# Performance work log

Measured on AMD Instinct MI355X. Metric: run time of the kernel, lower is better.

Reference implementation:

```python
import jax, jax.numpy as jnp
import numpy as np

EMBED_DIM = 1024
NUM_HEADS = 16
HEAD_DIM = EMBED_DIM // NUM_HEADS


def setup_inputs() -> dict:
    key = jax.random.key(0)
    k1, k2, k3, k4, k5 = jax.random.split(key, 5)
    B, S, D = 2, 2048, EMBED_DIM
    s_in = 1.0 / np.sqrt(D)
    x = jax.random.normal(k1, (B, S, D), dtype=jnp.float32)
    W_qkv = jax.random.uniform(k2, (D, 3 * D), dtype=jnp.float32, minval=-s_in, maxval=s_in)
    b_qkv = jax.random.uniform(k3, (3 * D,), dtype=jnp.float32, minval=-s_in, maxval=s_in)
    W_out = jax.random.uniform(k4, (D, D), dtype=jnp.float32, minval=-s_in, maxval=s_in)
    b_out = jax.random.uniform(k5, (D,), dtype=jnp.float32, minval=-s_in, maxval=s_in)
    return {"x": x, "W_qkv": W_qkv, "b_qkv": b_qkv, "W_out": W_out, "b_out": b_out}


def reference(x, W_qkv, b_qkv, W_out, b_out):
    B, S, D = x.shape
    H, Hd = NUM_HEADS, HEAD_DIM
    qkv = x @ W_qkv + b_qkv                      # [B,S,3D]
    qkv = qkv.reshape(B, S, 3, H, Hd)
    q = qkv[:, :, 0].transpose(0, 2, 1, 3)       # [B,H,S,Hd]
    k = qkv[:, :, 1].transpose(0, 2, 1, 3)
    v = qkv[:, :, 2].transpose(0, 2, 1, 3)
    scores = jnp.einsum('bhsd,bhtd->bhst', q, k) / jnp.sqrt(jnp.float32(Hd))
    attn = jax.nn.softmax(scores, axis=-1)       # dropout is identity in eval mode
    out = jnp.einsum('bhst,bhtd->bhsd', attn, v)
    out = out.transpose(0, 2, 1, 3).reshape(B, S, D)
    return out @ W_out + b_out
```

## Files before the change

kernel.cpp:

```cpp
#include <hip/hip_runtime.h>
#include <stdint.h>
#include <math.h>

#define EMBED 1024
#define HEADS 16
#define HDIM  64
#define SEQ   2048
#define BATCH 2

typedef __bf16 bf16x8 __attribute__((ext_vector_type(8)));
typedef float  f32x4  __attribute__((ext_vector_type(4)));
typedef unsigned short u16x8 __attribute__((ext_vector_type(8)));
typedef unsigned short u16x4 __attribute__((ext_vector_type(4)));
typedef uint32_t u32x4v __attribute__((ext_vector_type(4)));

static __device__ __forceinline__ unsigned short f2bf(float f){
  union { float f; uint32_t u; } v; v.f = f;
  uint32_t u = v.u;
  uint32_t r = (u + 0x7FFFu + ((u >> 16) & 1u)) >> 16;
  return (unsigned short)r;
}
static __device__ __forceinline__ bf16x8 as_bf(u16x8 v){ return __builtin_bit_cast(bf16x8, v); }

static __device__ __forceinline__ uint32_t pk_bf16(float a, float b){
#if defined(__has_builtin) && __has_builtin(__builtin_amdgcn_cvt_pk_bf16_f32)
  typedef __bf16 bf16x2 __attribute__((ext_vector_type(2)));
  bf16x2 p = __builtin_amdgcn_cvt_pk_bf16_f32(a, b);
  return __builtin_bit_cast(uint32_t, p);
#else
  return (uint32_t)f2bf(a) | ((uint32_t)f2bf(b) << 16);
#endif
}

static __device__ __forceinline__ float fexp2(float x){
#if defined(__has_builtin) && __has_builtin(__builtin_amdgcn_exp2f)
  return __builtin_amdgcn_exp2f(x);
#else
  return exp2f(x);
#endif
}

static __device__ __forceinline__ void stage16(const unsigned short* gp,
                                               unsigned short* lp_wave, int lane){
#if defined(__has_builtin) && __has_builtin(__builtin_amdgcn_global_load_lds)
  __builtin_amdgcn_global_load_lds((const __attribute__((address_space(1))) void*)gp,
                                   (__attribute__((address_space(3))) void*)lp_wave,
                                   16, 0, 0);
#else
  *(u16x8*)(lp_wave + lane * 8) = *(const u16x8*)gp;
#endif
}

__global__ __launch_bounds__(256) void prep(
    const float* __restrict__ x,      unsigned short* __restrict__ xb,
    const float* __restrict__ W_qkv,  unsigned short* __restrict__ wqkvT)
{
  __shared__ unsigned short T[32 * 36];
  const int bid = blockIdx.x;
  const int t   = threadIdx.x;

  if (bid < 4096){
    int i = (bid * 256 + t) * 4;
    float4 v = *(const float4*)(x + i);
    u16x4 o;
    o[0] = f2bf(v.x); o[1] = f2bf(v.y); o[2] = f2bf(v.z); o[3] = f2bf(v.w);
    *(u16x4*)(xb + i) = o;
    return;
  }
  int idx = bid - 4096;
  int n0 = (idx % 96) * 32, k0 = (idx / 96) * 32;
  int kr = t >> 3, nc = (t & 7) * 4;
  float4 wv = *(const float4*)(W_qkv + (size_t)(k0 + kr) * 3072 + n0 + nc);
  T[(nc + 0) * 36 + kr] = f2bf(wv.x);
  T[(nc + 1) * 36 + kr] = f2bf(wv.y);
  T[(nc + 2) * 36 + kr] = f2bf(wv.z);
  T[(nc + 3) * 36 + kr] = f2bf(wv.w);
  __syncthreads();
  int nr = t >> 3, kc = (t & 7) * 4;
  *(u16x4*)(wqkvT + (size_t)(n0 + nr) * 1024 + k0 + kc) = *(const u16x4*)&T[nr * 36 + kc];
}

__global__ __launch_bounds__(256) void wtrans_out(const float* __restrict__ W,
                                                  unsigned short* __restrict__ Wt){
  __shared__ unsigned short T[32 * 36];
  int t = threadIdx.x;
  int n0 = blockIdx.x * 32, k0 = blockIdx.y * 32;
  int kr = t >> 3, nc = (t & 7) * 4;
  float4 wv = *(const float4*)(W + (size_t)(k0 + kr) * 1024 + n0 + nc);
  T[(nc + 0) * 36 + kr] = f2bf(wv.x);
  T[(nc + 1) * 36 + kr] = f2bf(wv.y);
  T[(nc + 2) * 36 + kr] = f2bf(wv.z);
  T[(nc + 3) * 36 + kr] = f2bf(wv.w);
  __syncthreads();
  int nr = t >> 3, kc = (t & 7) * 4;
  *(u16x4*)(Wt + (size_t)(n0 + nr) * 1024 + k0 + kc) = *(const u16x4*)&T[nr * 36 + kc];
}

__global__ __launch_bounds__(256) void vtrans(const unsigned short* __restrict__ V,
                                              unsigned short* __restrict__ VT){
  __shared__ unsigned short T[32 * 36];
  int t = threadIdx.x;
  int s0 = blockIdx.x * 32, d0 = blockIdx.y * 32;
  size_t base = (size_t)blockIdx.z * SEQ * HDIM;
  int sr = t >> 3, dc = (t & 7) * 4;
  u16x4 vv = *(const u16x4*)(V + base + (size_t)(s0 + sr) * HDIM + d0 + dc);
  T[(dc + 0) * 36 + sr] = vv[0];
  T[(dc + 1) * 36 + sr] = vv[1];
  T[(dc + 2) * 36 + sr] = vv[2];
  T[(dc + 3) * 36 + sr] = vv[3];
  __syncthreads();
  int dr = t >> 3, sc = (t & 7) * 4;
  int pos = (((sc >> 2) & 3) << 3) + (((sc >> 4) & 1) << 2);
  *(u16x4*)(VT + base + (size_t)(d0 + dr) * SEQ + s0 + pos) = *(const u16x4*)&T[dr * 36 + sc];
}

__global__ __launch_bounds__(256) void gemm_qkv(
    const unsigned short* __restrict__ A,
    const unsigned short* __restrict__ Bt,
    const float* __restrict__ bias,
    unsigned short* __restrict__ q_ws,
    unsigned short* __restrict__ k_ws,
    unsigned short* __restrict__ v_ws,
    int M, int N, int K)
{
  __shared__ unsigned short As[128 * 32];
  __shared__ unsigned short Bs[128 * 32];
  const int tid  = threadIdx.x;
  const int bm   = blockIdx.y, bn = blockIdx.x;
  const int w    = tid >> 6, lane = tid & 63;
  const int quad = lane >> 4, l16 = lane & 15;
  const int wm   = (w >> 1) * 64, wn = (w & 1) * 64;

  f32x4 acc[4][4] = {};

  for (int k0 = 0; k0 < K; k0 += 32) {
    #pragma unroll
    for (int i = 0; i < 2; i++){
      int c = w + i * 4;
      int row = c * 16 + (lane >> 2);
      int kg = (lane & 3) ^ (row & 3);
      stage16(A  + (size_t)(bm * 128 + row) * K + k0 + kg * 8, &As[c * 512], lane);
      stage16(Bt + (size_t)(bn * 128 + row) * K + k0 + kg * 8, &Bs[c * 512], lane);
    }
    __syncthreads();

    bf16x8 af[4], bfr[4];
    #pragma unroll
    for (int t = 0; t < 4; t++){
      int ra = wm + t * 16 + l16;
      int rb = wn + t * 16 + l16;
      af[t]  = as_bf(*(const u16x8*)&As[(ra << 5) + ((quad ^ (ra & 3)) << 3)]);
      bfr[t] = as_bf(*(const u16x8*)&Bs[(rb << 5) + ((quad ^ (rb & 3)) << 3)]);
    }
    #pragma unroll
    for (int mt = 0; mt < 4; mt++)
      #pragma unroll
      for (int nt = 0; nt < 4; nt++)
        acc[mt][nt] = __builtin_amdgcn_mfma_f32_16x16x32_bf16(af[mt], bfr[nt], acc[mt][nt], 0, 0, 0);
    __syncthreads();
  }

  const int which = (bn * 128) >> 10;
  unsigned short* dst = (which == 0) ? q_ws : (which == 1) ? k_ws : v_ws;
  const float scale = (which == 0) ? 0.18033688f : 1.0f;
  const int b = bm >> 4;
  #pragma unroll
  for (int nt = 0; nt < 4; nt++){
    int gnb = bn * 128 + wn + nt * 16;
    int h   = (gnb & 1023) >> 6;
    int hd  = (gnb & 63) + l16;
    float bv = bias[gnb + l16];
    unsigned short* dp = dst + (size_t)(b * HEADS + h) * SEQ * HDIM + hd;
    #pragma unroll
    for (int mt = 0; mt < 4; mt++){
      int s0 = ((bm & 15) * 128) + wm + mt * 16 + quad * 4;
      #pragma unroll
      for (int r = 0; r < 4; r++)
        dp[(size_t)(s0 + r) * HDIM] = f2bf((acc[mt][nt][r] + bv) * scale);
    }
  }
}

__global__ __launch_bounds__(256) void gemm_out(
    const unsigned short* __restrict__ A,
    const unsigned short* __restrict__ Bt,
    const float* __restrict__ bias,
    float* __restrict__ Cout,
    int M, int N, int K)
{
  __shared__ unsigned short As[128 * 32];
  __shared__ unsigned short Bs[64 * 32];
  const int tid  = threadIdx.x;
  const int bm   = blockIdx.y, bn = blockIdx.x;
  const int w    = tid >> 6, lane = tid & 63;
  const int quad = lane >> 4, l16 = lane & 15;
  const int wm   = (w >> 1) * 64, wn = (w & 1) * 32;

  f32x4 acc[4][2] = {};

  for (int k0 = 0; k0 < K; k0 += 32) {
    #pragma unroll
    for (int i = 0; i < 2; i++){
      int c = w + i * 4;
      int row = c * 16 + (lane >> 2);
      int kg = (lane & 3) ^ (row & 3);
      stage16(A + (size_t)(bm * 128 + row) * K + k0 + kg * 8, &As[c * 512], lane);
    }
    {
      int c = w;
      int row = c * 16 + (lane >> 2);
      int kg = (lane & 3) ^ (row & 3);
      stage16(Bt + (size_t)(bn * 64 + row) * K + k0 + kg * 8, &Bs[c * 512], lane);
    }
    __syncthreads();

    bf16x8 af[4], bfr[2];
    #pragma unroll
    for (int t = 0; t < 4; t++){
      int ra = wm + t * 16 + l16;
      af[t] = as_bf(*(const u16x8*)&As[(ra << 5) + ((quad ^ (ra & 3)) << 3)]);
    }
    #pragma unroll
    for (int t = 0; t < 2; t++){
      int rb = wn + t * 16 + l16;
      bfr[t] = as_bf(*(const u16x8*)&Bs[(rb << 5) + ((quad ^ (rb & 3)) << 3)]);
    }
    #pragma unroll
    for (int mt = 0; mt < 4; mt++)
      #pragma unroll
      for (int nt = 0; nt < 2; nt++)
        acc[mt][nt] = __builtin_amdgcn_mfma_f32_16x16x32_bf16(af[mt], bfr[nt], acc[mt][nt], 0, 0, 0);
    __syncthreads();
  }

  #pragma unroll
  for (int mt = 0; mt < 4; mt++)
    #pragma unroll
    for (int nt = 0; nt < 2; nt++)
      #pragma unroll
      for (int r = 0; r < 4; r++){
        int gm = bm * 128 + wm + mt * 16 + quad * 4 + r;
        int gn = bn * 64 + wn + nt * 16 + l16;
        Cout[(size_t)gm * N + gn] = acc[mt][nt][r] + bias[gn];
      }
}

__global__ __launch_bounds__(512) void attn(
    const unsigned short* __restrict__ q_ws,
    const unsigned short* __restrict__ k_ws,
    const unsigned short* __restrict__ vt_ws,
    unsigned short* __restrict__ o_ws)
{
  __shared__ unsigned short Qs[256 * 64];
  __shared__ unsigned short Ks[2][64 * 64];
  __shared__ unsigned short VTs[2][64 * 64];
  const int tid  = threadIdx.x;
  const int qt   = blockIdx.x, bh = blockIdx.y;
  const int w    = tid >> 6, lane = tid & 63;
  const int quad = lane >> 4, l16 = lane & 15;
  const size_t base = (size_t)bh * SEQ * HDIM;

  #pragma unroll
  for (int i = 0; i < 4; i++){
    int c = w * 4 + i;
    int row = c * 8 + (lane >> 3);
    int kg = (lane & 7) ^ (row & 7);
    stage16(q_ws + base + (size_t)(qt * 256 + row) * HDIM + kg * 8, &Qs[c * 512], lane);
  }

  const int srow = w * 8 + (lane >> 3);
  const int skg  = (lane & 7) ^ (srow & 7);
  const int dofs = w * 512 + lane * 8;

  stage16(k_ws  + base + (size_t)srow * HDIM + skg * 8, &Ks[0][w * 512],  lane);
  stage16(vt_ws + base + (size_t)srow * SEQ + skg * 8,  &VTs[0][w * 512], lane);
  __syncthreads();

  bf16x8 bq[2][2];
  #pragma unroll
  for (int mq = 0; mq < 2; mq++){
    int row = w * 32 + mq * 16 + l16;
    #pragma unroll
    for (int ks = 0; ks < 2; ks++)
      bq[mq][ks] = as_bf(*(const u16x8*)&Qs[(row << 6) + ((((ks << 2) + quad) ^ (row & 7)) << 3)]);
  }

  const unsigned short* kp = k_ws  + base + (size_t)(64 + srow) * HDIM + skg * 8;
  const unsigned short* vp = vt_ws + base + (size_t)srow * SEQ + 64 + skg * 8;

  f32x4 acc[2][4] = {};
  float li[2] = {0.f, 0.f};

  for (int kt2 = 0; kt2 < SEQ / 128; kt2++){
    #pragma unroll
    for (int half = 0; half < 2; half++){
      const int cur = half;
      const int kt  = kt2 * 2 + half;
      u16x8 kpre, vpre;
      if (kt < SEQ / 64 - 1){
        kpre = *(const u16x8*)kp;  kp += 64 * HDIM;
        vpre = *(const u16x8*)vp;  vp += 64;
      }

      f32x4 sf[4][2] = {};
      #pragma unroll
      for (int ks = 0; ks < 2; ks++){
        #pragma unroll
        for (int nt = 0; nt < 4; nt++){
          int rk = nt * 16 + l16;
          bf16x8 ak = as_bf(*(const u16x8*)&Ks[cur][(rk << 6) + ((((ks << 2) + quad) ^ (rk & 7)) << 3)]);
          #pragma unroll
          for (int mq = 0; mq < 2; mq++)
            sf[nt][mq] = __builtin_amdgcn_mfma_f32_16x16x32_bf16(ak, bq[mq][ks], sf[nt][mq], 0, 0, 0);
        }
      }

      #pragma unroll
      for (int nt = 0; nt < 4; nt++)
        #pragma unroll
        for (int mq = 0; mq < 2; mq++)
          #pragma unroll
          for (int r = 0; r < 4; r++)
            sf[nt][mq][r] = fexp2(sf[nt][mq][r]);
      #pragma unroll
      for (int mq = 0; mq < 2; mq++)
        #pragma unroll
        for (int nt = 0; nt < 4; nt++)
          li[mq] += (sf[nt][mq][0] + sf[nt][mq][1]) + (sf[nt][mq][2] + sf[nt][mq][3]);

      #pragma unroll
      for (int c = 0; c < 2; c++){
        bf16x8 ap[2];
        #pragma unroll
        for (int mq = 0; mq < 2; mq++){
          u32x4v aw;
          aw[0] = pk_bf16(sf[c * 2][mq][0],     sf[c * 2][mq][1]);
          aw[1] = pk_bf16(sf[c * 2][mq][2],     sf[c * 2][mq][3]);
          aw[2] = pk_bf16(sf[c * 2 + 1][mq][0], sf[c * 2 + 1][mq][1]);
          aw[3] = pk_bf16(sf[c * 2 + 1][mq][2], sf[c * 2 + 1][mq][3]);
          ap[mq] = __builtin_bit_cast(bf16x8, aw);
        }
        #pragma unroll
        for (int nt = 0; nt < 4; nt++){
          int rv = nt * 16 + l16;
          bf16x8 bv = as_bf(*(const u16x8*)&VTs[cur][(rv << 6) + ((((c << 2) + quad) ^ (rv & 7)) << 3)]);
          #pragma unroll
          for (int mq = 0; mq < 2; mq++)
            acc[mq][nt] = __builtin_amdgcn_mfma_f32_16x16x32_bf16(ap[mq], bv, acc[mq][nt], 0, 0, 0);
        }
      }

      if (kt < SEQ / 64 - 1){
        *(u16x8*)&Ks[cur ^ 1][dofs]  = kpre;
        *(u16x8*)&VTs[cur ^ 1][dofs] = vpre;
      }
      __syncthreads();
    }
  }

  #pragma unroll
  for (int mq = 0; mq < 2; mq++){
    li[mq] += __shfl_xor(li[mq], 16);
    li[mq] += __shfl_xor(li[mq], 32);
  }
  float inv[2] = {1.0f / li[0], 1.0f / li[1]};
  float invr[2][4];
  #pragma unroll
  for (int mq = 0; mq < 2; mq++)
    #pragma unroll
    for (int r = 0; r < 4; r++)
      invr[mq][r] = __shfl(inv[mq], quad * 4 + r);

  int b = bh >> 4, h = bh & 15;
  #pragma unroll
  for (int mq = 0; mq < 2; mq++)
    #pragma unroll
    for (int nt = 0; nt < 4; nt++)
      #pragma unroll
      for (int r = 0; r < 4; r++){
        int s = qt * 256 + w * 32 + mq * 16 + quad * 4 + r;
        int d = h * 64 + nt * 16 + l16;
        o_ws[((size_t)(b * SEQ + s)) * EMBED + d] = f2bf(acc[mq][nt][r] * invr[mq][r]);
      }
}

extern "C" void kernel_launch(void* const* d_in, const int* in_sizes, int n_in,
                              void* d_out, int out_size, void* d_ws, size_t ws_size,
                              hipStream_t stream) {
  const float* x     = (const float*)d_in[0];
  const float* W_qkv = (const float*)d_in[1];
  const float* b_qkv = (const float*)d_in[2];
  const float* W_out = (const float*)d_in[3];
  const float* b_out = (const float*)d_in[4];
  float* out = (float*)d_out;

  char* ws = (char*)d_ws;
  unsigned short* xb    = (unsigned short*)(ws);
  unsigned short* q     = (unsigned short*)(ws + ((size_t)8  << 20));
  unsigned short* k     = (unsigned short*)(ws + ((size_t)16 << 20));
  unsigned short* v     = (unsigned short*)(ws + ((size_t)24 << 20));
  unsigned short* woutT = (unsigned short*)(ws + ((size_t)24 << 20));
  unsigned short* vt    = (unsigned short*)(ws + ((size_t)32 << 20));
  unsigned short* wqkvT = (unsigned short*)(ws + ((size_t)32 << 20));
  unsigned short* o     = xb;

  prep<<<dim3(7168), dim3(256), 0, stream>>>(x, xb, W_qkv, wqkvT);

  gemm_qkv<<<dim3(24, 32), dim3(256), 0, stream>>>(
      xb, wqkvT, b_qkv, q, k, v, 4096, 3072, 1024);

  vtrans<<<dim3(64, 2, 32), dim3(256), 0, stream>>>(v, vt);

  wtrans_out<<<dim3(32, 32), dim3(256), 0, stream>>>(W_out, woutT);

  attn<<<dim3(8, 32), dim3(512), 0, stream>>>(q, k, vt, o);

  gemm_out<<<dim3(16, 32), dim3(256), 0, stream>>>(
      o, woutT, b_out, out, 4096, 1024, 1024);
}
```

Baseline: 197.8 us.

## Fuse V transpose into QKV GEMM epilogue and W_out transpose into prep

Removes the separate vtrans and wtrans_out launches. The QKV GEMM now writes V directly in transposed, permuted layout through an LDS staging tile with XOR swizzle, and the prep kernel gains extra blocks that convert and transpose W_out. This saves two kernel launches and one global round trip of V, in exchange for a more complex epilogue and LDS reuse after the main loop.

Result: slower. 204.1 us (+3.2%).

```diff
diff --git a/kernel.cpp b/kernel.cpp
--- a/kernel.cpp
+++ b/kernel.cpp
@@ -53,7 +53,8 @@
 
 __global__ __launch_bounds__(256) void prep(
     const float* __restrict__ x,      unsigned short* __restrict__ xb,
-    const float* __restrict__ W_qkv,  unsigned short* __restrict__ wqkvT)
+    const float* __restrict__ W_qkv,  unsigned short* __restrict__ wqkvT,
+    const float* __restrict__ W_out,  unsigned short* __restrict__ woutT)
 {
   __shared__ unsigned short T[32 * 36];
   const int bid = blockIdx.x;
@@ -67,26 +68,18 @@
     *(u16x4*)(xb + i) = o;
     return;
   }
-  int idx = bid - 4096;
-  int n0 = (idx % 96) * 32, k0 = (idx / 96) * 32;
+  const float* W; unsigned short* Wt; int N, n0, k0;
+  if (bid < 7168){
+    int idx = bid - 4096;
+    W = W_qkv; Wt = wqkvT; N = 3072;
+    n0 = (idx % 96) * 32; k0 = (idx / 96) * 32;
+  } else {
+    int idx = bid - 7168;
+    W = W_out; Wt = woutT; N = 1024;
+    n0 = (idx & 31) * 32; k0 = (idx >> 5) * 32;
+  }
   int kr = t >> 3, nc = (t & 7) * 4;
-  float4 wv = *(const float4*)(W_qkv + (size_t)(k0 + kr) * 3072 + n0 + nc);
-  T[(nc + 0) * 36 + kr] = f2bf(wv.x);
-  T[(nc + 1) * 36 + kr] = f2bf(wv.y);
-  T[(nc + 2) * 36 + kr] = f2bf(wv.z);
-  T[(nc + 3) * 36 + kr] = f2bf(wv.w);
-  __syncthreads();
-  int nr = t >> 3, kc = (t & 7) * 4;
-  *(u16x4*)(wqkvT + (size_t)(n0 + nr) * 1024 + k0 + kc) = *(const u16x4*)&T[nr * 36 + kc];
-}
-
-__global__ __launch_bounds__(256) void wtrans_out(const float* __restrict__ W,
-                                                  unsigned short* __restrict__ Wt){
-  __shared__ unsigned short T[32 * 36];
-  int t = threadIdx.x;
-  int n0 = blockIdx.x * 32, k0 = blockIdx.y * 32;
-  int kr = t >> 3, nc = (t & 7) * 4;
-  float4 wv = *(const float4*)(W + (size_t)(k0 + kr) * 1024 + n0 + nc);
+  float4 wv = *(const float4*)(W + (size_t)(k0 + kr) * N + n0 + nc);
   T[(nc + 0) * 36 + kr] = f2bf(wv.x);
   T[(nc + 1) * 36 + kr] = f2bf(wv.y);
   T[(nc + 2) * 36 + kr] = f2bf(wv.z);
@@ -96,31 +89,13 @@
   *(u16x4*)(Wt + (size_t)(n0 + nr) * 1024 + k0 + kc) = *(const u16x4*)&T[nr * 36 + kc];
 }
 
-__global__ __launch_bounds__(256) void vtrans(const unsigned short* __restrict__ V,
-                                              unsigned short* __restrict__ VT){
-  __shared__ unsigned short T[32 * 36];
-  int t = threadIdx.x;
-  int s0 = blockIdx.x * 32, d0 = blockIdx.y * 32;
-  size_t base = (size_t)blockIdx.z * SEQ * HDIM;
-  int sr = t >> 3, dc = (t & 7) * 4;
-  u16x4 vv = *(const u16x4*)(V + base + (size_t)(s0 + sr) * HDIM + d0 + dc);
-  T[(dc + 0) * 36 + sr] = vv[0];
-  T[(dc + 1) * 36 + sr] = vv[1];
-  T[(dc + 2) * 36 + sr] = vv[2];
-  T[(dc + 3) * 36 + sr] = vv[3];
-  __syncthreads();
-  int dr = t >> 3, sc = (t & 7) * 4;
-  int pos = (((sc >> 2) & 3) << 3) + (((sc >> 4) & 1) << 2);
-  *(u16x4*)(VT + base + (size_t)(d0 + dr) * SEQ + s0 + pos) = *(const u16x4*)&T[dr * 36 + sc];
-}
-
 __global__ __launch_bounds__(256) void gemm_qkv(
     const unsigned short* __restrict__ A,
     const unsigned short* __restrict__ Bt,
     const float* __restrict__ bias,
     unsigned short* __restrict__ q_ws,
     unsigned short* __restrict__ k_ws,
-    unsigned short* __restrict__ v_ws,
+    unsigned short* __restrict__ vt_ws,
     int M, int N, int K)
 {
   __shared__ unsigned short As[128 * 32];
@@ -161,22 +136,57 @@
   }
 
   const int which = (bn * 128) >> 10;
-  unsigned short* dst = (which == 0) ? q_ws : (which == 1) ? k_ws : v_ws;
-  const float scale = (which == 0) ? 0.18033688f : 1.0f;
-  const int b = bm >> 4;
-  #pragma unroll
-  for (int nt = 0; nt < 4; nt++){
-    int gnb = bn * 128 + wn + nt * 16;
-    int h   = (gnb & 1023) >> 6;
-    int hd  = (gnb & 63) + l16;
-    float bv = bias[gnb + l16];
-    unsigned short* dp = dst + (size_t)(b * HEADS + h) * SEQ * HDIM + hd;
-    #pragma unroll
-    for (int mt = 0; mt < 4; mt++){
-      int s0 = ((bm & 15) * 128) + wm + mt * 16 + quad * 4;
-      #pragma unroll
-      for (int r = 0; r < 4; r++)
-        dp[(size_t)(s0 + r) * HDIM] = f2bf((acc[mt][nt][r] + bv) * scale);
+
+  if (which == 2){
+    unsigned short* T = (w < 2) ? &As[w * 2048] : &Bs[(w - 2) * 2048];
+    const int h = (bn - 16) * 2 + (wn >> 6);
+    const size_t bhbase = ((size_t)((bm >> 4) * HEADS + h)) * HDIM * SEQ;
+    const int sgbase = (bm & 15) * 128 + wm;
+    #pragma unroll
+    for (int p = 0; p < 2; p++){
+      #pragma unroll
+      for (int mi = 0; mi < 2; mi++){
+        int mt = p * 2 + mi;
+        #pragma unroll
+        for (int nt = 0; nt < 4; nt++){
+          float bv = bias[bn * 128 + wn + nt * 16 + l16];
+          uint32_t lo = pk_bf16(acc[mt][nt][0] + bv, acc[mt][nt][1] + bv);
+          uint32_t hi = pk_bf16(acc[mt][nt][2] + bv, acc[mt][nt][3] + bv);
+          int hd = nt * 16 + l16;
+          int qc = (quad * 2 + mi) ^ (hd & 7);
+          uint32_t* d2 = (uint32_t*)&T[hd * 32 + qc * 4];
+          d2[0] = lo; d2[1] = hi;
+        }
+      }
+      #pragma unroll
+      for (int i = 0; i < 4; i++){
+        int id = i * 64 + lane;
+        int hd = id >> 2, ch = id & 3;
+        int q0 = (ch * 2) ^ (hd & 7), q1 = (ch * 2 + 1) ^ (hd & 7);
+        const uint32_t* s0p = (const uint32_t*)&T[hd * 32 + q0 * 4];
+        const uint32_t* s1p = (const uint32_t*)&T[hd * 32 + q1 * 4];
+        u32x4v st; st[0] = s0p[0]; st[1] = s0p[1]; st[2] = s1p[0]; st[3] = s1p[1];
+        *(u32x4v*)(vt_ws + bhbase + (size_t)hd * SEQ + sgbase + p * 32 + ch * 8) = st;
+      }
+    }
+  } else {
+    unsigned short* dst = (which == 0) ? q_ws : k_ws;
+    const float scale = (which == 0) ? 0.18033688f : 1.0f;
+    const int b = bm >> 4;
+    #pragma unroll
+    for (int nt = 0; nt < 4; nt++){
+      int gnb = bn * 128 + wn + nt * 16;
+      int h   = (gnb & 1023) >> 6;
+      int hd  = (gnb & 63) + l16;
+      float bv = bias[gnb + l16];
+      unsigned short* dp = dst + (size_t)(b * HEADS + h) * SEQ * HDIM + hd;
+      #pragma unroll
+      for (int mt = 0; mt < 4; mt++){
+        int s0 = ((bm & 15) * 128) + wm + mt * 16 + quad * 4;
+        #pragma unroll
+        for (int r = 0; r < 4; r++)
+          dp[(size_t)(s0 + r) * HDIM] = f2bf((acc[mt][nt][r] + bv) * scale);
+      }
     }
   }
 }
@@ -398,20 +408,15 @@
   unsigned short* xb    = (unsigned short*)(ws);
   unsigned short* q     = (unsigned short*)(ws + ((size_t)8  << 20));
   unsigned short* k     = (unsigned short*)(ws + ((size_t)16 << 20));
-  unsigned short* v     = (unsigned short*)(ws + ((size_t)24 << 20));
-  unsigned short* woutT = (unsigned short*)(ws + ((size_t)24 << 20));
-  unsigned short* vt    = (unsigned short*)(ws + ((size_t)32 << 20));
+  unsigned short* vt    = (unsigned short*)(ws + ((size_t)24 << 20));
   unsigned short* wqkvT = (unsigned short*)(ws + ((size_t)32 << 20));
+  unsigned short* woutT = (unsigned short*)(ws + ((size_t)38 << 20));
   unsigned short* o     = xb;
 
-  prep<<<dim3(7168), dim3(256), 0, stream>>>(x, xb, W_qkv, wqkvT);
+  prep<<<dim3(8192), dim3(256), 0, stream>>>(x, xb, W_qkv, wqkvT, W_out, woutT);
 
   gemm_qkv<<<dim3(24, 32), dim3(256), 0, stream>>>(
-      xb, wqkvT, b_qkv, q, k, v, 4096, 3072, 1024);
-
-  vtrans<<<dim3(64, 2, 32), dim3(256), 0, stream>>>(v, vt);
-
-  wtrans_out<<<dim3(32, 32), dim3(256), 0, stream>>>(W_out, woutT);
+      xb, wqkvT, b_qkv, q, k, vt, 4096, 3072, 1024);
 
   attn<<<dim3(8, 32), dim3(512), 0, stream>>>(q, k, vt, o);
 
```
